# Optimization experiments

Measured on AMD Instinct MI355X. Metric: run time of the kernel, lower is better.

Reference implementation:

```python
import jax, jax.numpy as jnp
import numpy as np

D_MODEL, D_HIDDEN, N_EXPERTS, TOP_K = 1024, 2048, 8, 2


def setup_inputs() -> dict:
    key = jax.random.key(0)
    ks = jax.random.split(key, 8)
    s_in = 1.0 / np.sqrt(D_MODEL)
    s_hid = 1.0 / np.sqrt(D_HIDDEN)
    return {
        "x": jax.random.normal(ks[0], (1, 2048, D_MODEL), dtype=jnp.float32),
        # stacked expert weights, stored (in, out) so y = x @ W + b
        "W1": jax.random.normal(ks[1], (N_EXPERTS, D_MODEL, D_HIDDEN), dtype=jnp.float32) * s_in,
        "b1": jnp.zeros((N_EXPERTS, D_HIDDEN), dtype=jnp.float32),
        "W2": jax.random.normal(ks[2], (N_EXPERTS, D_MODEL, D_HIDDEN), dtype=jnp.float32) * s_in,
        "b2": jnp.zeros((N_EXPERTS, D_HIDDEN), dtype=jnp.float32),
        "Wo": jax.random.normal(ks[3], (N_EXPERTS, D_HIDDEN, D_MODEL), dtype=jnp.float32) * s_hid,
        "bo": jnp.zeros((N_EXPERTS, D_MODEL), dtype=jnp.float32),
        "Wr": jax.random.normal(ks[4], (D_MODEL, N_EXPERTS), dtype=jnp.float32) * s_in,
        "br": jnp.zeros((N_EXPERTS,), dtype=jnp.float32),
    }


def reference(x, W1, b1, W2, b2, Wo, bo, Wr, br):
    B, S, D = x.shape
    T = B * S
    xf = x.reshape(T, D)

    # router
    logits = xf @ Wr + br                      # [T, E]
    probs = jax.nn.softmax(logits, axis=-1)
    topk_probs, topk_idx = jax.lax.top_k(probs, TOP_K)  # [T, K]

    # combine weights: c[t, e] = sum_k topk_probs[t, k] * 1[topk_idx[t, k] == e]
    c = jnp.zeros((T, N_EXPERTS), dtype=xf.dtype)
    c = c.at[jnp.arange(T)[:, None], topk_idx].add(topk_probs)  # [T, E]

    # per-expert SwiGLU FFN applied densely, then masked-combined (same math
    # as the original gather/scatter loop since c[t,e]=0 for unrouted experts)
    h = jnp.einsum('td,edh->eth', xf, W1) + b1[:, None, :]   # [E, T, H]
    g = jnp.einsum('td,edh->eth', xf, W2) + b2[:, None, :]
    y = jnp.einsum('eth,ehd->etd', h * jax.nn.silu(g), Wo) + bo[:, None, :]
    out = jnp.einsum('etd,te->td', y, c).reshape(B, S, D)

    probs_mean = probs.mean(axis=0)
    lb_loss = (probs_mean * probs_mean).sum() * N_EXPERTS
    return out, lb_loss
```

## Files before the change

### kernel.cpp

```cpp
#include <hip/hip_runtime.h>
#include <hip/hip_bf16.h>

#define T_TOK 2048
#define DM 1024
#define DH 2048
#define NE 8
#define MT_MAX 40

using bf16x8 = __attribute__((ext_vector_type(8))) short;
using f32x4  = __attribute__((ext_vector_type(4))) float;

__device__ __forceinline__ unsigned short f2bf(float f) {
  union { float f; unsigned u; } v; v.f = f;
  unsigned r = v.u + 0x7FFFu + ((v.u >> 16) & 1u);
  return (unsigned short)(r >> 16);
}
__device__ __forceinline__ unsigned pk2(float a, float b) {
  return (unsigned)f2bf(a) | ((unsigned)f2bf(b) << 16);
}

#define GLOAD16(gsrc, ldst)                                                        \
  __builtin_amdgcn_global_load_lds(                                                \
      (const __attribute__((address_space(1))) unsigned int*)(gsrc),               \
      (__attribute__((address_space(3))) unsigned int*)(ldst), 16, 0, 0)

__global__ void k_init(int* __restrict__ cnt) {
  if (threadIdx.x < NE) cnt[threadIdx.x] = 0;
}

__global__ __launch_bounds__(256) void k_rconv(
    const float* __restrict__ x, const float* __restrict__ Wr, const float* __restrict__ br,
    int* __restrict__ cnt, int* __restrict__ idx, float* __restrict__ wgt,
    int* __restrict__ t2r, float* __restrict__ probs, unsigned short* __restrict__ xb,
    const float* __restrict__ W1, const float* __restrict__ W2, const float* __restrict__ Wo,
    unsigned short* __restrict__ W1T, unsigned short* __restrict__ W2T,
    unsigned short* __restrict__ WoT)
{
  __shared__ float t[64][65];
  if (blockIdx.x < 512) {
    const int wave = threadIdx.x >> 6, l = threadIdx.x & 63;
    const int tok = blockIdx.x * 4 + wave;
    float xv[16];
#pragma unroll
    for (int i = 0; i < 16; ++i) xv[i] = x[tok*DM + l + 64*i];
#pragma unroll
    for (int i = 0; i < 16; ++i) xb[tok*DM + l + 64*i] = f2bf(xv[i]);

    float acc[8] = {0.f,0.f,0.f,0.f,0.f,0.f,0.f,0.f};
#pragma unroll
    for (int i = 0; i < 16; ++i) {
      const float4* wp = (const float4*)&Wr[(size_t)(l + 64*i)*NE];
      float4 wa = wp[0], wb = wp[1];
      acc[0] += xv[i]*wa.x; acc[1] += xv[i]*wa.y; acc[2] += xv[i]*wa.z; acc[3] += xv[i]*wa.w;
      acc[4] += xv[i]*wb.x; acc[5] += xv[i]*wb.y; acc[6] += xv[i]*wb.z; acc[7] += xv[i]*wb.w;
    }
#pragma unroll
    for (int e = 0; e < 8; ++e) {
#pragma unroll
      for (int off = 32; off; off >>= 1) acc[e] += __shfl_xor(acc[e], off, 64);
      acc[e] += br[e];
    }
    float mx = acc[0];
#pragma unroll
    for (int e = 1; e < 8; ++e) mx = fmaxf(mx, acc[e]);
    float p[8], s = 0.f;
#pragma unroll
    for (int e = 0; e < 8; ++e) { p[e] = expf(acc[e] - mx); s += p[e]; }
    float inv = 1.f / s;
#pragma unroll
    for (int e = 0; e < 8; ++e) p[e] *= inv;

    int e0 = 0; float p0 = p[0];
#pragma unroll
    for (int e = 1; e < 8; ++e) if (p[e] > p0) { p0 = p[e]; e0 = e; }
    int e1 = -1; float p1 = -1.f;
#pragma unroll
    for (int e = 0; e < 8; ++e) { if (e == e0) continue; if (p[e] > p1) { p1 = p[e]; e1 = e; } }

    if (l == 0) {
#pragma unroll
      for (int e = 0; e < 8; ++e) probs[tok*NE + e] = p[e];
      int pos0 = atomicAdd(&cnt[e0], 1);
      idx[e0*T_TOK + pos0] = tok; wgt[e0*T_TOK + pos0] = p0;
      t2r[tok*2 + 0] = e0*T_TOK + pos0;
      int pos1 = atomicAdd(&cnt[e1], 1);
      idx[e1*T_TOK + pos1] = tok; wgt[e1*T_TOK + pos1] = p1;
      t2r[tok*2 + 1] = e1*T_TOK + pos1;
    }
    return;
  }

  int b = blockIdx.x - 512;
  const float* in; unsigned short* outT; int R, C;
  if (b < 4096)      { in = W1; outT = W1T; R = DM; C = DH; }
  else if (b < 8192) { in = W2; outT = W2T; R = DM; C = DH; b -= 4096; }
  else               { in = Wo; outT = WoT; R = DH; C = DM; b -= 8192; }
  const int nC = C / 64;
  const int tilesPerE = (R / 64) * nC;
  const int e  = b / tilesPerE;
  const int tb = b % tilesPerE;
  const int r0 = (tb / nC) * 64, c0 = (tb % nC) * 64;

  const int tid = threadIdx.x;
  const int lr = tid >> 4, lc = (tid & 15) * 4;
#pragma unroll
  for (int i = 0; i < 4; ++i) {
    float4 v = *(const float4*)&in[((size_t)e*R + r0 + lr + i*16)*C + c0 + lc];
    t[lr + i*16][lc+0] = v.x; t[lr + i*16][lc+1] = v.y;
    t[lr + i*16][lc+2] = v.z; t[lr + i*16][lc+3] = v.w;
  }
  __syncthreads();
  const int oc = tid >> 3;
  const int od = (tid & 7) * 8;
#pragma unroll
  for (int i = 0; i < 2; ++i) {
    int c = oc + i*32;
    uint4 v;
    v.x = pk2(t[od+0][c], t[od+1][c]);
    v.y = pk2(t[od+2][c], t[od+3][c]);
    v.z = pk2(t[od+4][c], t[od+5][c]);
    v.w = pk2(t[od+6][c], t[od+7][c]);
    *(uint4*)&outT[((size_t)e*C + c0 + c)*R + r0 + od] = v;
  }
}

__global__ __launch_bounds__(256) void k_finalize(
    const int* __restrict__ cnt, int* __restrict__ rb,
    const float* __restrict__ probs, float* __restrict__ out,
    int* __restrict__ MTp, int* __restrict__ mtab)
{
  __shared__ float red[8][256];
  const int tid = threadIdx.x;
  float s[8] = {0.f,0.f,0.f,0.f,0.f,0.f,0.f,0.f};
  for (int t = tid; t < T_TOK; t += 256) {
#pragma unroll
    for (int e = 0; e < 8; ++e) s[e] += probs[t*NE + e];
  }
#pragma unroll
  for (int e = 0; e < 8; ++e) red[e][tid] = s[e];
  __syncthreads();
  for (int w = 128; w > 0; w >>= 1) {
    if (tid < w) {
#pragma unroll
      for (int e = 0; e < 8; ++e) red[e][tid] += red[e][tid + w];
    }
    __syncthreads();
  }
  if (tid == 0) {
    float lb = 0.f;
#pragma unroll
    for (int e = 0; e < 8; ++e) {
      float mean = red[e][0] * (1.f / T_TOK);
      lb += mean * mean;
    }
    out[2097152] = lb * NE;
    int r = 0, mc = 0;
#pragma unroll
    for (int e = 0; e < 8; ++e) {
      rb[e] = r; r += cnt[e];
      int nmt = (cnt[e] + 127) / 128;
      for (int j = 0; j < nmt; ++j) mtab[mc++] = (e << 16) | j;
    }
    *MTp = mc;
  }
}

#define TM1 128
#define TN1 64
#define BKK 64

__global__ __launch_bounds__(256) void k_ffn1b(
    const unsigned short* __restrict__ xb,
    const unsigned short* __restrict__ W1T, const float* __restrict__ b1,
    const unsigned short* __restrict__ W2T, const float* __restrict__ b2,
    const int* __restrict__ cnt, const int* __restrict__ rbp,
    const int* __restrict__ idx, unsigned short* __restrict__ act,
    const int* __restrict__ MTp, const int* __restrict__ mtab)
{
  const int mtg = blockIdx.y;
  if (mtg >= *MTp) return;
  const int code = mtab[mtg];
  const int e = code >> 16, mt = code & 0xffff;
  const int Me = cnt[e];
  const int m0 = mt * TM1;
  const int nt = blockIdx.x;
  const int n0 = nt * TN1;

  __shared__ __align__(16) unsigned short As[TM1*BKK];
  __shared__ __align__(16) unsigned short Bh[TN1*BKK];
  __shared__ __align__(16) unsigned short Bg[TN1*BKK];
  __shared__ int toks[TM1];

  const int tid = threadIdx.x;
  if (tid < TM1) toks[tid] = idx[e*T_TOK + min(m0 + tid, Me - 1)];
  __syncthreads();

  const int lane = tid & 63;
  const int wave = tid >> 6;
  const int wm = wave >> 1, wn = wave & 1;
  const int row16 = lane & 15, kg = lane >> 4;
  const int sl = lane & 7;
  const int lr = lane >> 3;

  const unsigned short* asrc[4];
#pragma unroll
  for (int i = 0; i < 4; ++i) {
    int r = (wave*4 + i)*8 + lr;
    asrc[i] = &xb[(size_t)toks[r]*DM + ((sl ^ (r & 7)) * 8)];
  }
  const unsigned short *bsrc1[2], *bsrc2[2];
#pragma unroll
  for (int j = 0; j < 2; ++j) {
    int r = (wave*2 + j)*8 + lr;
    size_t gb = ((size_t)e*DH + n0 + r)*DM + ((sl ^ (r & 7)) * 8);
    bsrc1[j] = &W1T[gb]; bsrc2[j] = &W2T[gb];
  }

  f32x4 ah[4][2], ag[4][2];
#pragma unroll
  for (int i = 0; i < 4; ++i)
#pragma unroll
    for (int j = 0; j < 2; ++j) { ah[i][j] = 0.f; ag[i][j] = 0.f; }

  for (int k0 = 0; k0 < DM; k0 += BKK) {
#pragma unroll
    for (int i = 0; i < 4; ++i)
      GLOAD16(asrc[i] + k0, &As[(wave*4 + i)*512]);
#pragma unroll
    for (int j = 0; j < 2; ++j) {
      GLOAD16(bsrc1[j] + k0, &Bh[(wave*2 + j)*512]);
      GLOAD16(bsrc2[j] + k0, &Bg[(wave*2 + j)*512]);
    }
    __syncthreads();
#pragma unroll
    for (int ks = 0; ks < 2; ++ks) {
      const int kslot = ks*4 + kg;
      bf16x8 a[4], vbh[2], vbg[2];
#pragma unroll
      for (int mi = 0; mi < 4; ++mi) {
        int m = wm*64 + mi*16 + row16;
        a[mi] = *(const bf16x8*)&As[m*BKK + ((kslot ^ (m & 7)) * 8)];
      }
#pragma unroll
      for (int ni = 0; ni < 2; ++ni) {
        int n = wn*32 + ni*16 + row16;
        int off = n*BKK + ((kslot ^ (n & 7)) * 8);
        vbh[ni] = *(const bf16x8*)&Bh[off];
        vbg[ni] = *(const bf16x8*)&Bg[off];
      }
#pragma unroll
      for (int mi = 0; mi < 4; ++mi)
#pragma unroll
        for (int ni = 0; ni < 2; ++ni) {
          ah[mi][ni] = __builtin_amdgcn_mfma_f32_16x16x32_bf16(a[mi], vbh[ni], ah[mi][ni], 0, 0, 0);
          ag[mi][ni] = __builtin_amdgcn_mfma_f32_16x16x32_bf16(a[mi], vbg[ni], ag[mi][ni], 0, 0, 0);
        }
    }
    __syncthreads();
  }

  const int rb = rbp[e];
#pragma unroll
  for (int mi = 0; mi < 4; ++mi) {
#pragma unroll
    for (int i = 0; i < 4; ++i) {
      int rloc = wm*64 + mi*16 + (lane >> 4)*4 + i;
      int m = m0 + rloc;
      if (m < Me) {
#pragma unroll
        for (int ni = 0; ni < 2; ++ni) {
          int col = n0 + wn*32 + ni*16 + row16;
          float h = ah[mi][ni][i] + b1[e*DH + col];
          float g = ag[mi][ni][i] + b2[e*DH + col];
          float sg = g / (1.f + __expf(-g));
          act[(size_t)(rb + m)*DH + col] = f2bf(h * sg);
        }
      }
    }
  }
}

__global__ __launch_bounds__(256) void k_ffn2b(
    const unsigned short* __restrict__ act,
    const unsigned short* __restrict__ WoT, const float* __restrict__ bo,
    const int* __restrict__ cnt, const int* __restrict__ rbp,
    float* __restrict__ ys,
    const int* __restrict__ MTp, const int* __restrict__ mtab)
{
  const int mtg = blockIdx.y;
  if (mtg >= *MTp) return;
  const int code = mtab[mtg];
  const int e = code >> 16, mt = code & 0xffff;
  const int Me = cnt[e];
  const int m0 = mt * TM1;
  const int nt = blockIdx.x;
  const int n0 = nt * TN1;
  const int rb = rbp[e];

  __shared__ __align__(16) unsigned short As[TM1*BKK];
  __shared__ __align__(16) unsigned short Bs[TN1*BKK];

  const int tid = threadIdx.x;
  const int lane = tid & 63;
  const int wave = tid >> 6;
  const int wm = wave >> 1, wn = wave & 1;
  const int row16 = lane & 15, kg = lane >> 4;
  const int sl = lane & 7;
  const int lr = lane >> 3;

  const unsigned short* asrc[4];
#pragma unroll
  for (int i = 0; i < 4; ++i) {
    int r = (wave*4 + i)*8 + lr;
    int grow = rb + min(m0 + r, Me - 1);
    asrc[i] = &act[(size_t)grow*DH + ((sl ^ (r & 7)) * 8)];
  }
  const unsigned short* bsrc[2];
#pragma unroll
  for (int j = 0; j < 2; ++j) {
    int r = (wave*2 + j)*8 + lr;
    bsrc[j] = &WoT[((size_t)e*DM + n0 + r)*DH + ((sl ^ (r & 7)) * 8)];
  }

  f32x4 acc[4][2];
#pragma unroll
  for (int i = 0; i < 4; ++i)
#pragma unroll
    for (int j = 0; j < 2; ++j) acc[i][j] = 0.f;

  for (int k0 = 0; k0 < DH; k0 += BKK) {
#pragma unroll
    for (int i = 0; i < 4; ++i)
      GLOAD16(asrc[i] + k0, &As[(wave*4 + i)*512]);
#pragma unroll
    for (int j = 0; j < 2; ++j)
      GLOAD16(bsrc[j] + k0, &Bs[(wave*2 + j)*512]);
    __syncthreads();
#pragma unroll
    for (int ks = 0; ks < 2; ++ks) {
      const int kslot = ks*4 + kg;
      bf16x8 a[4], b[2];
#pragma unroll
      for (int mi = 0; mi < 4; ++mi) {
        int m = wm*64 + mi*16 + row16;
        a[mi] = *(const bf16x8*)&As[m*BKK + ((kslot ^ (m & 7)) * 8)];
      }
#pragma unroll
      for (int ni = 0; ni < 2; ++ni) {
        int n = wn*32 + ni*16 + row16;
        b[ni] = *(const bf16x8*)&Bs[n*BKK + ((kslot ^ (n & 7)) * 8)];
      }
#pragma unroll
      for (int mi = 0; mi < 4; ++mi)
#pragma unroll
        for (int ni = 0; ni < 2; ++ni)
          acc[mi][ni] = __builtin_amdgcn_mfma_f32_16x16x32_bf16(a[mi], b[ni], acc[mi][ni], 0, 0, 0);
    }
    __syncthreads();
  }

#pragma unroll
  for (int mi = 0; mi < 4; ++mi) {
#pragma unroll
    for (int i = 0; i < 4; ++i) {
      int rloc = wm*64 + mi*16 + (lane >> 4)*4 + i;
      int m = m0 + rloc;
      if (m < Me) {
#pragma unroll
        for (int ni = 0; ni < 2; ++ni) {
          int col = n0 + wn*32 + ni*16 + row16;
          ys[(size_t)(rb + m)*DM + col] = acc[mi][ni][i] + bo[e*DM + col];
        }
      }
    }
  }
}

__global__ __launch_bounds__(256) void k_combine(
    const float* __restrict__ ys, const int* __restrict__ t2r,
    const int* __restrict__ rbp, const float* __restrict__ wgt,
    float* __restrict__ out)
{
  const int t = blockIdx.x, tid = threadIdx.x;
  const int c0 = t2r[t*2 + 0], c1 = t2r[t*2 + 1];
  const float w0 = wgt[c0], w1 = wgt[c1];
  const int r0 = rbp[c0 >> 11] + (c0 & 2047);
  const int r1 = rbp[c1 >> 11] + (c1 & 2047);
  const float4* p0 = (const float4*)&ys[(size_t)r0*DM];
  const float4* p1 = (const float4*)&ys[(size_t)r1*DM];
  float4* po = (float4*)&out[(size_t)t*DM];
  float4 a = p0[tid], b = p1[tid];
  float4 r;
  r.x = w0*a.x + w1*b.x; r.y = w0*a.y + w1*b.y;
  r.z = w0*a.z + w1*b.z; r.w = w0*a.w + w1*b.w;
  po[tid] = r;
}

extern "C" void kernel_launch(void* const* d_in, const int* in_sizes, int n_in,
                              void* d_out, int out_size, void* d_ws, size_t ws_size,
                              hipStream_t stream)
{
  const float* x  = (const float*)d_in[0];
  const float* W1 = (const float*)d_in[1];
  const float* b1 = (const float*)d_in[2];
  const float* W2 = (const float*)d_in[3];
  const float* b2 = (const float*)d_in[4];
  const float* Wo = (const float*)d_in[5];
  const float* bo = (const float*)d_in[6];
  const float* Wr = (const float*)d_in[7];
  const float* br = (const float*)d_in[8];
  float* out = (float*)d_out;

  char* ws = (char*)d_ws;
  int*   cnt   = (int*)(ws + 0);
  int*   rb    = (int*)(ws + 64);
  int*   MTp   = (int*)(ws + 128);
  int*   mtab  = (int*)(ws + 192);
  int*   t2r   = (int*)(ws + 4096);
  int*   idx   = (int*)(ws + 32*1024);
  float* wgt   = (float*)(ws + 96*1024);
  float* probs = (float*)(ws + 160*1024);
  unsigned short* xb  = (unsigned short*)(ws + 256*1024);
  unsigned short* act = (unsigned short*)(ws + 5ull*1024*1024);
  float* ysb = (float*)(ws + 21ull*1024*1024);
  unsigned short* W1T = (unsigned short*)(ws + 40ull*1024*1024);
  unsigned short* W2T = (unsigned short*)(ws + 72ull*1024*1024);
  unsigned short* WoT = (unsigned short*)(ws + 104ull*1024*1024);

  k_init<<<1, 64, 0, stream>>>(cnt);
  k_rconv<<<512 + 12288, 256, 0, stream>>>(x, Wr, br, cnt, idx, wgt, t2r, probs, xb,
                                           W1, W2, Wo, W1T, W2T, WoT);
  k_finalize<<<1, 256, 0, stream>>>(cnt, rb, probs, out, MTp, mtab);
  k_ffn1b<<<dim3(DH/TN1, MT_MAX), 256, 0, stream>>>(xb, W1T, b1, W2T, b2, cnt, rb, idx, act, MTp, mtab);
  k_ffn2b<<<dim3(DM/TN1, MT_MAX), 256, 0, stream>>>(act, WoT, bo, cnt, rb, ysb, MTp, mtab);
  k_combine<<<T_TOK, 256, 0, stream>>>(ysb, t2r, rb, wgt, out);
}
```

Before: 213.9 us.

## Rework weight transpose-convert with bf16 swizzled LDS tiles and four tiles per block

The weight transpose/convert path now packs fp32 to bf16 before writing to shared memory, using an XOR-swizzled 128-byte-row layout in place of a padded fp32 tile. Each block handles four 64x64 tiles with double-buffered LDS, cutting the grid from 12288 to 3072 conversion blocks. The goals are less LDS traffic and fewer bank conflicts, 16-byte vector LDS reads, and lower block launch overhead. Because the two LDS buffers alternate, reusing one two tiles later relies on the barrier in the intervening iteration.

```diff
diff --git a/kernel.cpp b/kernel.cpp
--- a/kernel.cpp
+++ b/kernel.cpp
@@ -28,7 +28,7 @@
   if (threadIdx.x < NE) cnt[threadIdx.x] = 0;
 }
 
-__global__ __launch_bounds__(256) void k_rconv(
+__global__ __launch_bounds__(256) void k_wconv(
     const float* __restrict__ x, const float* __restrict__ Wr, const float* __restrict__ br,
     int* __restrict__ cnt, int* __restrict__ idx, float* __restrict__ wgt,
     int* __restrict__ t2r, float* __restrict__ probs, unsigned short* __restrict__ xb,
@@ -36,9 +36,11 @@
     unsigned short* __restrict__ W1T, unsigned short* __restrict__ W2T,
     unsigned short* __restrict__ WoT)
 {
-  __shared__ float t[64][65];
+  __shared__ __align__(16) unsigned short tb[2][64*64];
+  const int tid = threadIdx.x;
+
   if (blockIdx.x < 512) {
-    const int wave = threadIdx.x >> 6, l = threadIdx.x & 63;
+    const int wave = tid >> 6, l = tid & 63;
     const int tok = blockIdx.x * 4 + wave;
     float xv[16];
 #pragma unroll
@@ -90,37 +92,48 @@
     return;
   }
 
-  int b = blockIdx.x - 512;
-  const float* in; unsigned short* outT; int R, C;
-  if (b < 4096)      { in = W1; outT = W1T; R = DM; C = DH; }
-  else if (b < 8192) { in = W2; outT = W2T; R = DM; C = DH; b -= 4096; }
-  else               { in = Wo; outT = WoT; R = DH; C = DM; b -= 8192; }
-  const int nC = C / 64;
-  const int tilesPerE = (R / 64) * nC;
-  const int e  = b / tilesPerE;
-  const int tb = b % tilesPerE;
-  const int r0 = (tb / nC) * 64, c0 = (tb % nC) * 64;
-
-  const int tid = threadIdx.x;
-  const int lr = tid >> 4, lc = (tid & 15) * 4;
-#pragma unroll
-  for (int i = 0; i < 4; ++i) {
-    float4 v = *(const float4*)&in[((size_t)e*R + r0 + lr + i*16)*C + c0 + lc];
-    t[lr + i*16][lc+0] = v.x; t[lr + i*16][lc+1] = v.y;
-    t[lr + i*16][lc+2] = v.z; t[lr + i*16][lc+3] = v.w;
-  }
-  __syncthreads();
-  const int oc = tid >> 3;
-  const int od = (tid & 7) * 8;
-#pragma unroll
-  for (int i = 0; i < 2; ++i) {
-    int c = oc + i*32;
-    uint4 v;
-    v.x = pk2(t[od+0][c], t[od+1][c]);
-    v.y = pk2(t[od+2][c], t[od+3][c]);
-    v.z = pk2(t[od+4][c], t[od+5][c]);
-    v.w = pk2(t[od+6][c], t[od+7][c]);
-    *(uint4*)&outT[((size_t)e*C + c0 + c)*R + r0 + od] = v;
+  const int bx = tid >> 4;
+  const int by = tid & 15;
+  const int rn = tid >> 3;
+  const int sl8 = tid & 7;
+
+#pragma unroll
+  for (int it = 0; it < 4; ++it) {
+    int tt = (blockIdx.x - 512) * 4 + it;
+    const float* in; unsigned short* outT; int nCs;
+    int R, C;
+    if (tt < 4096)      { in = W1; outT = W1T; R = DM; C = DH; nCs = 5; }
+    else if (tt < 8192) { in = W2; outT = W2T; R = DM; C = DH; nCs = 5; tt -= 4096; }
+    else                { in = Wo; outT = WoT; R = DH; C = DM; nCs = 4; tt -= 8192; }
+    const int e  = tt >> 9;
+    const int te = tt & 511;
+    const int r0 = (te >> nCs) << 6;
+    const int c0 = (te & ((1 << nCs) - 1)) << 6;
+
+    float4 v[4];
+#pragma unroll
+    for (int i = 0; i < 4; ++i)
+      v[i] = *(const float4*)&in[((size_t)e*R + r0 + bx*4 + i)*C + c0 + by*4];
+
+    unsigned short* B = tb[it & 1];
+#pragma unroll
+    for (int j = 0; j < 4; ++j) {
+      int n = by*4 + j;
+      uint2 w;
+      w.x = pk2(((const float*)&v[0])[j], ((const float*)&v[1])[j]);
+      w.y = pk2(((const float*)&v[2])[j], ((const float*)&v[3])[j]);
+      int byteoff = n*128 + (((bx >> 1) ^ ((n >> 2) & 7)) * 16) + (bx & 1) * 8;
+      *(uint2*)((char*)B + byteoff) = w;
+    }
+    __syncthreads();
+
+#pragma unroll
+    for (int h = 0; h < 2; ++h) {
+      int n = rn + h*32;
+      int byteoff = n*128 + ((sl8 ^ ((n >> 2) & 7)) * 16);
+      uint4 w = *(const uint4*)((const char*)B + byteoff);
+      *(uint4*)&outT[((size_t)e*C + c0 + n)*R + r0 + sl8*8] = w;
+    }
   }
 }
 
@@ -428,8 +441,8 @@
   unsigned short* WoT = (unsigned short*)(ws + 104ull*1024*1024);
 
   k_init<<<1, 64, 0, stream>>>(cnt);
-  k_rconv<<<512 + 12288, 256, 0, stream>>>(x, Wr, br, cnt, idx, wgt, t2r, probs, xb,
-                                           W1, W2, Wo, W1T, W2T, WoT);
+  k_wconv<<<512 + 3072, 256, 0, stream>>>(x, Wr, br, cnt, idx, wgt, t2r, probs, xb,
+                                          W1, W2, Wo, W1T, W2T, WoT);
   k_finalize<<<1, 256, 0, stream>>>(cnt, rb, probs, out, MTp, mtab);
   k_ffn1b<<<dim3(DH/TN1, MT_MAX), 256, 0, stream>>>(xb, W1T, b1, W2T, b2, cnt, rb, idx, act, MTp, mtab);
   k_ffn2b<<<dim3(DM/TN1, MT_MAX), 256, 0, stream>>>(act, WoT, bo, cnt, rb, ysb, MTp, mtab);
```

After: 219.4 us. 2.5% more time.

## Fuse weight transpose and bf16 conversion into expert GEMM tile loads

Applied to the files above, without the earlier changes.

Drops the separate pass that transposed and converted all fp32 expert weights to bf16 before the GEMMs. Each FFN GEMM now loads fp32 weight tiles straight into registers, packs them to bf16, and writes them transposed into swizzled LDS, using a new two-level XOR swizzle for bank spreading. This removes a full write and re-read of the converted weights. In exchange, each M-tile now reads fp32 weights, which is twice the bytes of bf16 per reread, and these register-staged loads no longer use the asynchronous global-to-LDS path.

```diff
diff --git a/kernel.cpp b/kernel.cpp
--- a/kernel.cpp
+++ b/kernel.cpp
@@ -19,6 +19,8 @@
   return (unsigned)f2bf(a) | ((unsigned)f2bf(b) << 16);
 }
 
+#define SW(n) ((((n) & 7)) ^ (((n) >> 3) & 7))
+
 #define GLOAD16(gsrc, ldst)                                                        \
   __builtin_amdgcn_global_load_lds(                                                \
       (const __attribute__((address_space(1))) unsigned int*)(gsrc),               \
@@ -28,99 +30,59 @@
   if (threadIdx.x < NE) cnt[threadIdx.x] = 0;
 }
 
-__global__ __launch_bounds__(256) void k_rconv(
+__global__ __launch_bounds__(256) void k_router(
     const float* __restrict__ x, const float* __restrict__ Wr, const float* __restrict__ br,
     int* __restrict__ cnt, int* __restrict__ idx, float* __restrict__ wgt,
-    int* __restrict__ t2r, float* __restrict__ probs, unsigned short* __restrict__ xb,
-    const float* __restrict__ W1, const float* __restrict__ W2, const float* __restrict__ Wo,
-    unsigned short* __restrict__ W1T, unsigned short* __restrict__ W2T,
-    unsigned short* __restrict__ WoT)
-{
-  __shared__ float t[64][65];
-  if (blockIdx.x < 512) {
-    const int wave = threadIdx.x >> 6, l = threadIdx.x & 63;
-    const int tok = blockIdx.x * 4 + wave;
-    float xv[16];
-#pragma unroll
-    for (int i = 0; i < 16; ++i) xv[i] = x[tok*DM + l + 64*i];
-#pragma unroll
-    for (int i = 0; i < 16; ++i) xb[tok*DM + l + 64*i] = f2bf(xv[i]);
-
-    float acc[8] = {0.f,0.f,0.f,0.f,0.f,0.f,0.f,0.f};
-#pragma unroll
-    for (int i = 0; i < 16; ++i) {
-      const float4* wp = (const float4*)&Wr[(size_t)(l + 64*i)*NE];
-      float4 wa = wp[0], wb = wp[1];
-      acc[0] += xv[i]*wa.x; acc[1] += xv[i]*wa.y; acc[2] += xv[i]*wa.z; acc[3] += xv[i]*wa.w;
-      acc[4] += xv[i]*wb.x; acc[5] += xv[i]*wb.y; acc[6] += xv[i]*wb.z; acc[7] += xv[i]*wb.w;
-    }
-#pragma unroll
-    for (int e = 0; e < 8; ++e) {
-#pragma unroll
-      for (int off = 32; off; off >>= 1) acc[e] += __shfl_xor(acc[e], off, 64);
-      acc[e] += br[e];
-    }
-    float mx = acc[0];
-#pragma unroll
-    for (int e = 1; e < 8; ++e) mx = fmaxf(mx, acc[e]);
-    float p[8], s = 0.f;
-#pragma unroll
-    for (int e = 0; e < 8; ++e) { p[e] = expf(acc[e] - mx); s += p[e]; }
-    float inv = 1.f / s;
-#pragma unroll
-    for (int e = 0; e < 8; ++e) p[e] *= inv;
-
-    int e0 = 0; float p0 = p[0];
-#pragma unroll
-    for (int e = 1; e < 8; ++e) if (p[e] > p0) { p0 = p[e]; e0 = e; }
-    int e1 = -1; float p1 = -1.f;
-#pragma unroll
-    for (int e = 0; e < 8; ++e) { if (e == e0) continue; if (p[e] > p1) { p1 = p[e]; e1 = e; } }
-
-    if (l == 0) {
-#pragma unroll
-      for (int e = 0; e < 8; ++e) probs[tok*NE + e] = p[e];
-      int pos0 = atomicAdd(&cnt[e0], 1);
-      idx[e0*T_TOK + pos0] = tok; wgt[e0*T_TOK + pos0] = p0;
-      t2r[tok*2 + 0] = e0*T_TOK + pos0;
-      int pos1 = atomicAdd(&cnt[e1], 1);
-      idx[e1*T_TOK + pos1] = tok; wgt[e1*T_TOK + pos1] = p1;
-      t2r[tok*2 + 1] = e1*T_TOK + pos1;
-    }
-    return;
-  }
-
-  int b = blockIdx.x - 512;
-  const float* in; unsigned short* outT; int R, C;
-  if (b < 4096)      { in = W1; outT = W1T; R = DM; C = DH; }
-  else if (b < 8192) { in = W2; outT = W2T; R = DM; C = DH; b -= 4096; }
-  else               { in = Wo; outT = WoT; R = DH; C = DM; b -= 8192; }
-  const int nC = C / 64;
-  const int tilesPerE = (R / 64) * nC;
-  const int e  = b / tilesPerE;
-  const int tb = b % tilesPerE;
-  const int r0 = (tb / nC) * 64, c0 = (tb % nC) * 64;
-
-  const int tid = threadIdx.x;
-  const int lr = tid >> 4, lc = (tid & 15) * 4;
-#pragma unroll
-  for (int i = 0; i < 4; ++i) {
-    float4 v = *(const float4*)&in[((size_t)e*R + r0 + lr + i*16)*C + c0 + lc];
-    t[lr + i*16][lc+0] = v.x; t[lr + i*16][lc+1] = v.y;
-    t[lr + i*16][lc+2] = v.z; t[lr + i*16][lc+3] = v.w;
-  }
-  __syncthreads();
-  const int oc = tid >> 3;
-  const int od = (tid & 7) * 8;
-#pragma unroll
-  for (int i = 0; i < 2; ++i) {
-    int c = oc + i*32;
-    uint4 v;
-    v.x = pk2(t[od+0][c], t[od+1][c]);
-    v.y = pk2(t[od+2][c], t[od+3][c]);
-    v.z = pk2(t[od+4][c], t[od+5][c]);
-    v.w = pk2(t[od+6][c], t[od+7][c]);
-    *(uint4*)&outT[((size_t)e*C + c0 + c)*R + r0 + od] = v;
+    int* __restrict__ t2r, float* __restrict__ probs, unsigned short* __restrict__ xb)
+{
+  const int wave = threadIdx.x >> 6, l = threadIdx.x & 63;
+  const int t = blockIdx.x * 4 + wave;
+  float xv[16];
+#pragma unroll
+  for (int i = 0; i < 16; ++i) xv[i] = x[t*DM + l + 64*i];
+#pragma unroll
+  for (int i = 0; i < 16; ++i) xb[t*DM + l + 64*i] = f2bf(xv[i]);
+
+  float acc[8] = {0.f,0.f,0.f,0.f,0.f,0.f,0.f,0.f};
+#pragma unroll
+  for (int i = 0; i < 16; ++i) {
+    const float4* wp = (const float4*)&Wr[(size_t)(l + 64*i)*NE];
+    float4 wa = wp[0], wb = wp[1];
+    acc[0] += xv[i]*wa.x; acc[1] += xv[i]*wa.y; acc[2] += xv[i]*wa.z; acc[3] += xv[i]*wa.w;
+    acc[4] += xv[i]*wb.x; acc[5] += xv[i]*wb.y; acc[6] += xv[i]*wb.z; acc[7] += xv[i]*wb.w;
+  }
+#pragma unroll
+  for (int e = 0; e < 8; ++e) {
+#pragma unroll
+    for (int off = 32; off; off >>= 1) acc[e] += __shfl_xor(acc[e], off, 64);
+    acc[e] += br[e];
+  }
+  float mx = acc[0];
+#pragma unroll
+  for (int e = 1; e < 8; ++e) mx = fmaxf(mx, acc[e]);
+  float p[8], s = 0.f;
+#pragma unroll
+  for (int e = 0; e < 8; ++e) { p[e] = expf(acc[e] - mx); s += p[e]; }
+  float inv = 1.f / s;
+#pragma unroll
+  for (int e = 0; e < 8; ++e) p[e] *= inv;
+
+  int e0 = 0; float p0 = p[0];
+#pragma unroll
+  for (int e = 1; e < 8; ++e) if (p[e] > p0) { p0 = p[e]; e0 = e; }
+  int e1 = -1; float p1 = -1.f;
+#pragma unroll
+  for (int e = 0; e < 8; ++e) { if (e == e0) continue; if (p[e] > p1) { p1 = p[e]; e1 = e; } }
+
+  if (l == 0) {
+#pragma unroll
+    for (int e = 0; e < 8; ++e) probs[t*NE + e] = p[e];
+    int pos0 = atomicAdd(&cnt[e0], 1);
+    idx[e0*T_TOK + pos0] = t; wgt[e0*T_TOK + pos0] = p0;
+    t2r[t*2 + 0] = e0*T_TOK + pos0;
+    int pos1 = atomicAdd(&cnt[e1], 1);
+    idx[e1*T_TOK + pos1] = t; wgt[e1*T_TOK + pos1] = p1;
+    t2r[t*2 + 1] = e1*T_TOK + pos1;
   }
 }
 
@@ -171,8 +133,8 @@
 
 __global__ __launch_bounds__(256) void k_ffn1b(
     const unsigned short* __restrict__ xb,
-    const unsigned short* __restrict__ W1T, const float* __restrict__ b1,
-    const unsigned short* __restrict__ W2T, const float* __restrict__ b2,
+    const float* __restrict__ W1, const float* __restrict__ b1,
+    const float* __restrict__ W2, const float* __restrict__ b2,
     const int* __restrict__ cnt, const int* __restrict__ rbp,
     const int* __restrict__ idx, unsigned short* __restrict__ act,
     const int* __restrict__ MTp, const int* __restrict__ mtab)
@@ -208,13 +170,12 @@
     int r = (wave*4 + i)*8 + lr;
     asrc[i] = &xb[(size_t)toks[r]*DM + ((sl ^ (r & 7)) * 8)];
   }
-  const unsigned short *bsrc1[2], *bsrc2[2];
-#pragma unroll
-  for (int j = 0; j < 2; ++j) {
-    int r = (wave*2 + j)*8 + lr;
-    size_t gb = ((size_t)e*DH + n0 + r)*DM + ((sl ^ (r & 7)) * 8);
-    bsrc1[j] = &W1T[gb]; bsrc2[j] = &W2T[gb];
-  }
+
+  const int nq = tid & 15;
+  const int kq = tid >> 4;
+  const float* w1p = W1 + ((size_t)e*DM + kq*4)*DH + n0 + nq*4;
+  const float* w2p = W2 + ((size_t)e*DM + kq*4)*DH + n0 + nq*4;
+  const int bunit = kq >> 1, bhalf = (kq & 1) * 8;
 
   f32x4 ah[4][2], ag[4][2];
 #pragma unroll
@@ -223,13 +184,27 @@
     for (int j = 0; j < 2; ++j) { ah[i][j] = 0.f; ag[i][j] = 0.f; }
 
   for (int k0 = 0; k0 < DM; k0 += BKK) {
+    const float* p1 = w1p + (size_t)k0 * DH;
+    const float* p2 = w2p + (size_t)k0 * DH;
+    float4 v1[4], v2[4];
+#pragma unroll
+    for (int i = 0; i < 4; ++i) v1[i] = *(const float4*)(p1 + (size_t)i*DH);
+#pragma unroll
+    for (int i = 0; i < 4; ++i) v2[i] = *(const float4*)(p2 + (size_t)i*DH);
 #pragma unroll
     for (int i = 0; i < 4; ++i)
       GLOAD16(asrc[i] + k0, &As[(wave*4 + i)*512]);
-#pragma unroll
-    for (int j = 0; j < 2; ++j) {
-      GLOAD16(bsrc1[j] + k0, &Bh[(wave*2 + j)*512]);
-      GLOAD16(bsrc2[j] + k0, &Bg[(wave*2 + j)*512]);
+    const float* f1 = (const float*)v1;
+    const float* f2 = (const float*)v2;
+#pragma unroll
+    for (int j = 0; j < 4; ++j) {
+      const int n = nq*4 + j;
+      const int bo = n*128 + ((bunit ^ SW(n)) * 16) + bhalf;
+      uint2 w1v, w2v;
+      w1v.x = pk2(f1[0*4+j], f1[1*4+j]); w1v.y = pk2(f1[2*4+j], f1[3*4+j]);
+      w2v.x = pk2(f2[0*4+j], f2[1*4+j]); w2v.y = pk2(f2[2*4+j], f2[3*4+j]);
+      *(uint2*)((char*)Bh + bo) = w1v;
+      *(uint2*)((char*)Bg + bo) = w2v;
     }
     __syncthreads();
 #pragma unroll
@@ -244,7 +219,7 @@
 #pragma unroll
       for (int ni = 0; ni < 2; ++ni) {
         int n = wn*32 + ni*16 + row16;
-        int off = n*BKK + ((kslot ^ (n & 7)) * 8);
+        int off = n*BKK + ((kslot ^ SW(n)) * 8);
         vbh[ni] = *(const bf16x8*)&Bh[off];
         vbg[ni] = *(const bf16x8*)&Bg[off];
       }
@@ -282,7 +257,7 @@
 
 __global__ __launch_bounds__(256) void k_ffn2b(
     const unsigned short* __restrict__ act,
-    const unsigned short* __restrict__ WoT, const float* __restrict__ bo,
+    const float* __restrict__ Wo, const float* __restrict__ bo,
     const int* __restrict__ cnt, const int* __restrict__ rbp,
     float* __restrict__ ys,
     const int* __restrict__ MTp, const int* __restrict__ mtab)
@@ -315,12 +290,11 @@
     int grow = rb + min(m0 + r, Me - 1);
     asrc[i] = &act[(size_t)grow*DH + ((sl ^ (r & 7)) * 8)];
   }
-  const unsigned short* bsrc[2];
-#pragma unroll
-  for (int j = 0; j < 2; ++j) {
-    int r = (wave*2 + j)*8 + lr;
-    bsrc[j] = &WoT[((size_t)e*DM + n0 + r)*DH + ((sl ^ (r & 7)) * 8)];
-  }
+
+  const int nq = tid & 15;
+  const int kq = tid >> 4;
+  const float* wop = Wo + ((size_t)e*DH + kq*4)*DM + n0 + nq*4;
+  const int bunit = kq >> 1, bhalf = (kq & 1) * 8;
 
   f32x4 acc[4][2];
 #pragma unroll
@@ -329,12 +303,22 @@
     for (int j = 0; j < 2; ++j) acc[i][j] = 0.f;
 
   for (int k0 = 0; k0 < DH; k0 += BKK) {
+    const float* p1 = wop + (size_t)k0 * DM;
+    float4 v1[4];
+#pragma unroll
+    for (int i = 0; i < 4; ++i) v1[i] = *(const float4*)(p1 + (size_t)i*DM);
 #pragma unroll
     for (int i = 0; i < 4; ++i)
       GLOAD16(asrc[i] + k0, &As[(wave*4 + i)*512]);
-#pragma unroll
-    for (int j = 0; j < 2; ++j)
-      GLOAD16(bsrc[j] + k0, &Bs[(wave*2 + j)*512]);
+    const float* f1 = (const float*)v1;
+#pragma unroll
+    for (int j = 0; j < 4; ++j) {
+      const int n = nq*4 + j;
+      const int bo = n*128 + ((bunit ^ SW(n)) * 16) + bhalf;
+      uint2 w1v;
+      w1v.x = pk2(f1[0*4+j], f1[1*4+j]); w1v.y = pk2(f1[2*4+j], f1[3*4+j]);
+      *(uint2*)((char*)Bs + bo) = w1v;
+    }
     __syncthreads();
 #pragma unroll
     for (int ks = 0; ks < 2; ++ks) {
@@ -348,7 +332,7 @@
 #pragma unroll
       for (int ni = 0; ni < 2; ++ni) {
         int n = wn*32 + ni*16 + row16;
-        b[ni] = *(const bf16x8*)&Bs[n*BKK + ((kslot ^ (n & 7)) * 8)];
+        b[ni] = *(const bf16x8*)&Bs[n*BKK + ((kslot ^ SW(n)) * 8)];
       }
 #pragma unroll
       for (int mi = 0; mi < 4; ++mi)
@@ -423,15 +407,11 @@
   unsigned short* xb  = (unsigned short*)(ws + 256*1024);
   unsigned short* act = (unsigned short*)(ws + 5ull*1024*1024);
   float* ysb = (float*)(ws + 21ull*1024*1024);
-  unsigned short* W1T = (unsigned short*)(ws + 40ull*1024*1024);
-  unsigned short* W2T = (unsigned short*)(ws + 72ull*1024*1024);
-  unsigned short* WoT = (unsigned short*)(ws + 104ull*1024*1024);
 
   k_init<<<1, 64, 0, stream>>>(cnt);
-  k_rconv<<<512 + 12288, 256, 0, stream>>>(x, Wr, br, cnt, idx, wgt, t2r, probs, xb,
-                                           W1, W2, Wo, W1T, W2T, WoT);
+  k_router<<<T_TOK/4, 256, 0, stream>>>(x, Wr, br, cnt, idx, wgt, t2r, probs, xb);
   k_finalize<<<1, 256, 0, stream>>>(cnt, rb, probs, out, MTp, mtab);
-  k_ffn1b<<<dim3(DH/TN1, MT_MAX), 256, 0, stream>>>(xb, W1T, b1, W2T, b2, cnt, rb, idx, act, MTp, mtab);
-  k_ffn2b<<<dim3(DM/TN1, MT_MAX), 256, 0, stream>>>(act, WoT, bo, cnt, rb, ysb, MTp, mtab);
+  k_ffn1b<<<dim3(DH/TN1, MT_MAX), 256, 0, stream>>>(xb, W1, b1, W2, b2, cnt, rb, idx, act, MTp, mtab);
+  k_ffn2b<<<dim3(DM/TN1, MT_MAX), 256, 0, stream>>>(act, Wo, bo, cnt, rb, ysb, MTp, mtab);
   k_combine<<<T_TOK, 256, 0, stream>>>(ysb, t2r, rb, wgt, out);
 }
```

Result: no change. 212.1 us (-0.8%).
